# Optimization experiments

Hardware: AMD Instinct MI355X
Metric: run time of the kernel (lower is better)

Reference implementation:

```python
import jax, jax.numpy as jnp
import numpy as np

D = 128          # embed_dim
N = 400000       # rows in each source state buffer (h_bot/c_bot and h_buf/c_buf)
K = 200000       # gathers per source per child side (M = 2*K merge targets)


def setup_inputs() -> dict:
    key = jax.random.key(0)
    ks = jax.random.split(key, 10)
    h_bot = jax.random.normal(ks[0], (N, D), dtype=jnp.float32)
    c_bot = jax.random.normal(ks[1], (N, D), dtype=jnp.float32)
    h_buf = jax.random.normal(ks[2], (N, D), dtype=jnp.float32)
    c_buf = jax.random.normal(ks[3], (N, D), dtype=jnp.float32)
    bot_from_l = jax.random.randint(ks[4], (K,), 0, N, dtype=jnp.int32)
    prev_from_l = jax.random.randint(ks[5], (K,), 0, N, dtype=jnp.int32)
    bot_from_r = jax.random.randint(ks[6], (K,), 0, N, dtype=jnp.int32)
    prev_from_r = jax.random.randint(ks[7], (K,), 0, N, dtype=jnp.int32)
    # BinaryTreeLSTMCell params: 5 gates (i, o, u, f_l, f_r) over [h_l; h_r]
    W = jax.random.normal(ks[8], (2 * D, 5 * D), dtype=jnp.float32) * (1.0 / np.sqrt(2 * D))
    b = jnp.zeros((5 * D,), dtype=jnp.float32)
    return {"h_bot": h_bot, "c_bot": c_bot, "h_buf": h_buf, "c_buf": c_buf,
            "bot_from_l": bot_from_l, "prev_from_l": prev_from_l,
            "bot_from_r": bot_from_r, "prev_from_r": prev_from_r,
            "W": W, "b": b}


def _multi_select(bot_src, prev_src, bot_from, prev_from):
    # multi_index_select with 'to' ids in concat order: gather rows from the two
    # source buffers into the [M, D] merge-target buffer.
    return jnp.concatenate([bot_src[bot_from], prev_src[prev_from]], axis=0)


def _binary_tree_lstm_cell(h_l, c_l, h_r, c_r, W, b):
    # N-ary (N=2) TreeLSTM merge cell, no input x.
    gates = jnp.concatenate([h_l, h_r], axis=1) @ W + b  # [M, 5D]
    i, o, u, f_l, f_r = jnp.split(gates, 5, axis=1)
    c = jax.nn.sigmoid(i) * jnp.tanh(u) \
        + jax.nn.sigmoid(f_l) * c_l + jax.nn.sigmoid(f_r) * c_r
    h = jax.nn.sigmoid(o) * jnp.tanh(c)
    return h, c


def reference(h_bot, c_bot, h_buf, c_buf,
              bot_from_l, prev_from_l, bot_from_r, prev_from_r, W, b):
    # batch_tree_lstm2: tree_state_select gathers for left and right children,
    # then one BinaryTreeLSTMCell merge over all M targets.
    h_l = _multi_select(h_bot, h_buf, bot_from_l, prev_from_l)
    c_l = _multi_select(c_bot, c_buf, bot_from_l, prev_from_l)
    h_r = _multi_select(h_bot, h_buf, bot_from_r, prev_from_r)
    c_r = _multi_select(c_bot, c_buf, bot_from_r, prev_from_r)
    h, c = _binary_tree_lstm_cell(h_l, c_l, h_r, c_r, W, b)
    return jnp.stack([h, c])  # [2, M, D]
```

## Files before the change

kernel.cpp:

```cpp
#include <hip/hip_runtime.h>

typedef __attribute__((ext_vector_type(8))) short short8_t;
typedef __attribute__((ext_vector_type(4))) float f32x4_t;

#define DDIM 128
#define BM   64
#define LDA  264

__device__ __forceinline__ unsigned short f2bf(float x) {
  union { float f; unsigned u; } v; v.f = x;
  unsigned r = v.u + 0x7FFFu + ((v.u >> 16) & 1u);
  return (unsigned short)(r >> 16);
}

__device__ __forceinline__ float sigf(float x) {
  return 1.0f / (1.0f + __expf(-x));
}
__device__ __forceinline__ float tanh_fast(float x) {
  return 2.0f / (1.0f + __expf(-2.0f * x)) - 1.0f;
}

__global__ void convert_w_kernel(const float* __restrict__ W,
                                 unsigned short* __restrict__ Wt,
                                 int twoD, int fiveD) {
  const int c = blockIdx.x;
  const int k = threadIdx.x;
  Wt[c * twoD + k] = f2bf(W[k * fiveD + c]);
}

__global__ __launch_bounds__(512)
void treelstm_fused_kernel(const float* __restrict__ h_bot,
                           const float* __restrict__ c_bot,
                           const float* __restrict__ h_buf,
                           const float* __restrict__ c_buf,
                           const int* __restrict__ idx_bl,
                           const int* __restrict__ idx_pl,
                           const int* __restrict__ idx_br,
                           const int* __restrict__ idx_pr,
                           const float* __restrict__ bias,
                           const unsigned short* __restrict__ Wt,
                           float* __restrict__ out,
                           int K, int M) {
  __shared__ __align__(16) unsigned short A_lds[BM * LDA];

  const int tid   = threadIdx.x;
  const int mbase = blockIdx.x * BM;
  if (mbase >= M) return;

  const int wave = tid >> 6;
  const int lane = tid & 63;
  const int l16  = lane & 15;
  const int lq   = lane >> 4;
  const int d0   = wave * 16 + lq * 4;

  const int r    = tid >> 3;
  const int seg  = tid & 7;
  const int half = seg >> 2;
  const int cs   = seg & 3;
  const int ms   = mbase + r;

  float4 hv[8];
  {
    int hidx; const float* hsrc;
    if (half == 0) {
      if (ms < K) { hidx = idx_bl[ms];     hsrc = h_bot; }
      else        { hidx = idx_pl[ms - K]; hsrc = h_buf; }
    } else {
      if (ms < K) { hidx = idx_br[ms];     hsrc = h_bot; }
      else        { hidx = idx_pr[ms - K]; hsrc = h_buf; }
    }
    const float4* s4 = (const float4*)(hsrc + (size_t)hidx * DDIM);
    #pragma unroll
    for (int q = 0; q < 8; ++q) hv[q] = s4[cs + 4 * q];
  }

  f32x4_t cl[4], cr[4], bs[5];
  int mvec[4];
  #pragma unroll
  for (int mt = 0; mt < 4; ++mt) {
    const int m = mbase + mt * 16 + l16;
    mvec[mt] = m;
    int il, ir; const float *cls, *crs;
    if (m < K) { il = idx_bl[m];     cls = c_bot; }
    else       { il = idx_pl[m - K]; cls = c_buf; }
    if (m < K) { ir = idx_br[m];     crs = c_bot; }
    else       { ir = idx_pr[m - K]; crs = c_buf; }
    cl[mt] = *(const f32x4_t*)(cls + (size_t)il * DDIM + d0);
    cr[mt] = *(const f32x4_t*)(crs + (size_t)ir * DDIM + d0);
  }
  #pragma unroll
  for (int g = 0; g < 5; ++g)
    bs[g] = *(const f32x4_t*)(bias + g * DDIM + d0);

  {
    unsigned short* dst = &A_lds[r * LDA + half * DDIM];
    #pragma unroll
    for (int q = 0; q < 8; ++q) {
      ushort4 w;
      w.x = f2bf(hv[q].x); w.y = f2bf(hv[q].y);
      w.z = f2bf(hv[q].z); w.w = f2bf(hv[q].w);
      *(ushort4*)(dst + (cs + 4 * q) * 4) = w;
    }
  }
  __syncthreads();

  f32x4_t acc[4][5];
  #pragma unroll
  for (int mt = 0; mt < 4; ++mt)
    #pragma unroll
    for (int g = 0; g < 5; ++g) {
      f32x4_t z = {0.0f, 0.0f, 0.0f, 0.0f};
      acc[mt][g] = z;
    }

  const unsigned short* wb = Wt + (size_t)(wave * 16 + l16) * 256 + lq * 8;
  const int ab = l16 * LDA + lq * 8;

  #pragma unroll
  for (int kk = 0; kk < 8; ++kk) {
    const int k0 = kk * 32;
    short8_t wf[5];
    #pragma unroll
    for (int g = 0; g < 5; ++g)
      wf[g] = *(const short8_t*)(wb + (size_t)g * (128 * 256) + k0);
    short8_t hf[4];
    #pragma unroll
    for (int mt = 0; mt < 4; ++mt)
      hf[mt] = *(const short8_t*)(&A_lds[ab + mt * (16 * LDA) + k0]);
    #pragma unroll
    for (int g = 0; g < 5; ++g)
      #pragma unroll
      for (int mt = 0; mt < 4; ++mt)
        acc[mt][g] = __builtin_amdgcn_mfma_f32_16x16x32_bf16(
            wf[g], hf[mt], acc[mt][g], 0, 0, 0);
  }

  float* __restrict__ out_h = out;
  float* __restrict__ out_c = out + (size_t)M * DDIM;

  #pragma unroll
  for (int mt = 0; mt < 4; ++mt) {
    f32x4_t hv4, cv4;
    #pragma unroll
    for (int j = 0; j < 4; ++j) {
      const float gi = acc[mt][0][j] + bs[0][j];
      const float go = acc[mt][1][j] + bs[1][j];
      const float gu = acc[mt][2][j] + bs[2][j];
      const float gl = acc[mt][3][j] + bs[3][j];
      const float gr = acc[mt][4][j] + bs[4][j];
      const float cn = sigf(gi) * tanh_fast(gu)
                     + sigf(gl) * cl[mt][j] + sigf(gr) * cr[mt][j];
      const float hn = sigf(go) * tanh_fast(cn);
      cv4[j] = cn; hv4[j] = hn;
    }
    const size_t off = (size_t)mvec[mt] * DDIM + d0;
    *(f32x4_t*)(out_h + off) = hv4;
    *(f32x4_t*)(out_c + off) = cv4;
  }
}

extern "C" void kernel_launch(void* const* d_in, const int* in_sizes, int n_in,
                              void* d_out, int out_size, void* d_ws, size_t ws_size,
                              hipStream_t stream) {
  const float* h_bot  = (const float*)d_in[0];
  const float* c_bot  = (const float*)d_in[1];
  const float* h_buf  = (const float*)d_in[2];
  const float* c_buf  = (const float*)d_in[3];
  const int*   idx_bl = (const int*)d_in[4];
  const int*   idx_pl = (const int*)d_in[5];
  const int*   idx_br = (const int*)d_in[6];
  const int*   idx_pr = (const int*)d_in[7];
  const float* W      = (const float*)d_in[8];
  const float* bias   = (const float*)d_in[9];

  const int K = in_sizes[4];
  const int M = 2 * K;
  const int fiveD = in_sizes[9];
  const int twoD  = in_sizes[8] / fiveD;

  unsigned short* Wt = (unsigned short*)d_ws;

  hipLaunchKernelGGL(convert_w_kernel, dim3(fiveD), dim3(twoD), 0, stream,
                     W, Wt, twoD, fiveD);

  const int grid = (M + BM - 1) / BM;
  hipLaunchKernelGGL(treelstm_fused_kernel, dim3(grid), dim3(512), 0, stream,
                     h_bot, c_bot, h_buf, c_buf,
                     idx_bl, idx_pl, idx_br, idx_pr,
                     bias, Wt, (float*)d_out, K, M);
}
```

Before: 536.9 us.

## Make fused TreeLSTM kernel persistent with prefetched gathers and swizzled LDS

Replaces the one-tile-per-block launch with a persistent grid of 512 blocks of 256 threads, each looping over 32-row tiles. The next tile's h rows are gathered into registers while the current tile's MFMAs run, then written to LDS after a barrier. The padded LDS layout becomes an XOR-swizzled layout, and sigmoid/tanh use the hardware reciprocal instead of division. The aim is to hide gather latency and cut launch/tail costs. In exchange, the fixed grid of 512 blocks may underfill the GPU, W fragments are reloaded per tile, and each row pays extra barriers.

```diff
diff --git a/kernel.cpp b/kernel.cpp
--- a/kernel.cpp
+++ b/kernel.cpp
@@ -4,8 +4,8 @@
 typedef __attribute__((ext_vector_type(4))) float f32x4_t;
 
 #define DDIM 128
-#define BM   64
-#define LDA  264
+#define BM   32
+#define ROWB 512
 
 __device__ __forceinline__ unsigned short f2bf(float x) {
   union { float f; unsigned u; } v; v.f = x;
@@ -14,10 +14,10 @@
 }
 
 __device__ __forceinline__ float sigf(float x) {
-  return 1.0f / (1.0f + __expf(-x));
+  return __builtin_amdgcn_rcpf(1.0f + __expf(-x));
 }
 __device__ __forceinline__ float tanh_fast(float x) {
-  return 2.0f / (1.0f + __expf(-2.0f * x)) - 1.0f;
+  return 2.0f * __builtin_amdgcn_rcpf(1.0f + __expf(-2.0f * x)) - 1.0f;
 }
 
 __global__ void convert_w_kernel(const float* __restrict__ W,
@@ -28,7 +28,7 @@
   Wt[c * twoD + k] = f2bf(W[k * fiveD + c]);
 }
 
-__global__ __launch_bounds__(512)
+__global__ __launch_bounds__(256)
 void treelstm_fused_kernel(const float* __restrict__ h_bot,
                            const float* __restrict__ c_bot,
                            const float* __restrict__ h_buf,
@@ -40,123 +40,168 @@
                            const float* __restrict__ bias,
                            const unsigned short* __restrict__ Wt,
                            float* __restrict__ out,
-                           int K, int M) {
-  __shared__ __align__(16) unsigned short A_lds[BM * LDA];
-
-  const int tid   = threadIdx.x;
-  const int mbase = blockIdx.x * BM;
-  if (mbase >= M) return;
-
-  const int wave = tid >> 6;
+                           int K, int M, int ntiles) {
+  __shared__ __align__(16) char A_lds[BM * ROWB];
+
+  const int tid = threadIdx.x;
+
+  const int sr    = tid >> 3;
+  const int seg   = tid & 7;
+  const int shalf = seg >> 2;
+  const int scs   = seg & 3;
+  char* const sdst = A_lds + sr * ROWB;
+  const int sswz  = (sr & 7) << 4;
+
+  const int w    = tid >> 6;
   const int lane = tid & 63;
   const int l16  = lane & 15;
   const int lq   = lane >> 4;
-  const int d0   = wave * 16 + lq * 4;
-
-  const int r    = tid >> 3;
-  const int seg  = tid & 7;
-  const int half = seg >> 2;
-  const int cs   = seg & 3;
-  const int ms   = mbase + r;
-
-  float4 hv[8];
+  const int rswz = (l16 & 7) << 4;
+
+  float* const out_h = out;
+  float* const out_c = out + (size_t)M * DDIM;
+
+  int t = blockIdx.x;
+  const int stride = gridDim.x;
+  if (t >= ntiles) return;
+
+#define LOAD_H(tt, hv)                                                   \
+  {                                                                      \
+    const int ms = (tt) * BM + sr;                                       \
+    int hidx = 0; const float* hsrc;                                     \
+    if (shalf == 0) {                                                    \
+      if (ms < K) { hidx = idx_bl[ms]; hsrc = h_bot; }                   \
+      else        { hidx = (ms < M) ? idx_pl[ms - K] : 0; hsrc = h_buf; }\
+    } else {                                                             \
+      if (ms < K) { hidx = idx_br[ms]; hsrc = h_bot; }                   \
+      else        { hidx = (ms < M) ? idx_pr[ms - K] : 0; hsrc = h_buf; }\
+    }                                                                    \
+    const float4* s4 = (const float4*)(hsrc + (size_t)hidx * DDIM);      \
+    _Pragma("unroll")                                                    \
+    for (int q = 0; q < 8; ++q) hv[q] = s4[scs + 4 * q];                 \
+  }
+
+#define WRITE_H(hv)                                                      \
+  {                                                                      \
+    _Pragma("unroll")                                                    \
+    for (int q = 0; q < 8; ++q) {                                        \
+      const int f4i = scs + 4 * q;                                       \
+      ushort4 u;                                                         \
+      u.x = f2bf(hv[q].x); u.y = f2bf(hv[q].y);                          \
+      u.z = f2bf(hv[q].z); u.w = f2bf(hv[q].w);                          \
+      const int byt = (shalf * 256 + f4i * 8) ^ sswz;                    \
+      *(ushort4*)(sdst + byt) = u;                                       \
+    }                                                                    \
+  }
+
   {
-    int hidx; const float* hsrc;
-    if (half == 0) {
-      if (ms < K) { hidx = idx_bl[ms];     hsrc = h_bot; }
-      else        { hidx = idx_pl[ms - K]; hsrc = h_buf; }
-    } else {
-      if (ms < K) { hidx = idx_br[ms];     hsrc = h_bot; }
-      else        { hidx = idx_pr[ms - K]; hsrc = h_buf; }
+    float4 hv[8];
+    LOAD_H(t, hv);
+    WRITE_H(hv);
+  }
+  __syncthreads();
+
+  for (;;) {
+    const int tn = t + stride;
+    const bool more = (tn < ntiles);
+
+    float4 hv2[8];
+    if (more) LOAD_H(tn, hv2);
+
+    const int tb = t * BM;
+    int mvec[2];
+    f32x4_t cl[2][2], cr[2][2];
+    #pragma unroll
+    for (int mt = 0; mt < 2; ++mt) {
+      const int m = tb + mt * 16 + l16;
+      mvec[mt] = m;
+      const int mm = (m < M) ? m : 0;
+      int il, ir; const float *cls, *crs;
+      if (mm < K) { il = idx_bl[mm];     cls = c_bot; }
+      else        { il = idx_pl[mm - K]; cls = c_buf; }
+      if (mm < K) { ir = idx_br[mm];     crs = c_bot; }
+      else        { ir = idx_pr[mm - K]; crs = c_buf; }
+      #pragma unroll
+      for (int dtb = 0; dtb < 2; ++dtb) {
+        const int d0 = dtb * 64 + w * 16 + lq * 4;
+        cl[mt][dtb] = *(const f32x4_t*)(cls + (size_t)il * DDIM + d0);
+        cr[mt][dtb] = *(const f32x4_t*)(crs + (size_t)ir * DDIM + d0);
+      }
     }
-    const float4* s4 = (const float4*)(hsrc + (size_t)hidx * DDIM);
-    #pragma unroll
-    for (int q = 0; q < 8; ++q) hv[q] = s4[cs + 4 * q];
-  }
-
-  f32x4_t cl[4], cr[4], bs[5];
-  int mvec[4];
-  #pragma unroll
-  for (int mt = 0; mt < 4; ++mt) {
-    const int m = mbase + mt * 16 + l16;
-    mvec[mt] = m;
-    int il, ir; const float *cls, *crs;
-    if (m < K) { il = idx_bl[m];     cls = c_bot; }
-    else       { il = idx_pl[m - K]; cls = c_buf; }
-    if (m < K) { ir = idx_br[m];     crs = c_bot; }
-    else       { ir = idx_pr[m - K]; crs = c_buf; }
-    cl[mt] = *(const f32x4_t*)(cls + (size_t)il * DDIM + d0);
-    cr[mt] = *(const f32x4_t*)(crs + (size_t)ir * DDIM + d0);
-  }
-  #pragma unroll
-  for (int g = 0; g < 5; ++g)
-    bs[g] = *(const f32x4_t*)(bias + g * DDIM + d0);
-
-  {
-    unsigned short* dst = &A_lds[r * LDA + half * DDIM];
-    #pragma unroll
-    for (int q = 0; q < 8; ++q) {
-      ushort4 w;
-      w.x = f2bf(hv[q].x); w.y = f2bf(hv[q].y);
-      w.z = f2bf(hv[q].z); w.w = f2bf(hv[q].w);
-      *(ushort4*)(dst + (cs + 4 * q) * 4) = w;
+
+    f32x4_t acc[2][2][5];
+    #pragma unroll
+    for (int mt = 0; mt < 2; ++mt)
+      #pragma unroll
+      for (int dtb = 0; dtb < 2; ++dtb)
+        #pragma unroll
+        for (int g = 0; g < 5; ++g) {
+          f32x4_t z = {0.0f, 0.0f, 0.0f, 0.0f};
+          acc[mt][dtb][g] = z;
+        }
+
+    #pragma unroll
+    for (int kk = 0; kk < 8; ++kk) {
+      short8_t hf[2];
+      #pragma unroll
+      for (int mt = 0; mt < 2; ++mt) {
+        const int byt = (lq * 16 + kk * 64) ^ rswz;
+        hf[mt] = *(const short8_t*)(A_lds + (mt * 16 + l16) * ROWB + byt);
+      }
+      #pragma unroll
+      for (int dtb = 0; dtb < 2; ++dtb)
+        #pragma unroll
+        for (int g = 0; g < 5; ++g) {
+          const int c = g * 128 + dtb * 64 + w * 16 + l16;
+          const short8_t wf =
+              *(const short8_t*)(Wt + (size_t)c * 256 + lq * 8 + kk * 32);
+          #pragma unroll
+          for (int mt = 0; mt < 2; ++mt)
+            acc[mt][dtb][g] = __builtin_amdgcn_mfma_f32_16x16x32_bf16(
+                wf, hf[mt], acc[mt][dtb][g], 0, 0, 0);
+        }
     }
-  }
-  __syncthreads();
-
-  f32x4_t acc[4][5];
-  #pragma unroll
-  for (int mt = 0; mt < 4; ++mt)
-    #pragma unroll
-    for (int g = 0; g < 5; ++g) {
-      f32x4_t z = {0.0f, 0.0f, 0.0f, 0.0f};
-      acc[mt][g] = z;
+
+    __syncthreads();
+    if (more) { WRITE_H(hv2); }
+
+    #pragma unroll
+    for (int mt = 0; mt < 2; ++mt) {
+      if (mvec[mt] < M) {
+        #pragma unroll
+        for (int dtb = 0; dtb < 2; ++dtb) {
+          const int d0 = dtb * 64 + w * 16 + lq * 4;
+          f32x4_t bv[5];
+          #pragma unroll
+          for (int g = 0; g < 5; ++g)
+            bv[g] = *(const f32x4_t*)(bias + g * DDIM + d0);
+          f32x4_t hv4, cv4;
+          #pragma unroll
+          for (int j = 0; j < 4; ++j) {
+            const float gi = acc[mt][dtb][0][j] + bv[0][j];
+            const float go = acc[mt][dtb][1][j] + bv[1][j];
+            const float gu = acc[mt][dtb][2][j] + bv[2][j];
+            const float gl = acc[mt][dtb][3][j] + bv[3][j];
+            const float gr = acc[mt][dtb][4][j] + bv[4][j];
+            const float cn = sigf(gi) * tanh_fast(gu)
+                           + sigf(gl) * cl[mt][dtb][j]
+                           + sigf(gr) * cr[mt][dtb][j];
+            const float hn = sigf(go) * tanh_fast(cn);
+            cv4[j] = cn; hv4[j] = hn;
+          }
+          const size_t off = (size_t)mvec[mt] * DDIM + d0;
+          *(f32x4_t*)(out_h + off) = hv4;
+          *(f32x4_t*)(out_c + off) = cv4;
+        }
+      }
     }
 
-  const unsigned short* wb = Wt + (size_t)(wave * 16 + l16) * 256 + lq * 8;
-  const int ab = l16 * LDA + lq * 8;
-
-  #pragma unroll
-  for (int kk = 0; kk < 8; ++kk) {
-    const int k0 = kk * 32;
-    short8_t wf[5];
-    #pragma unroll
-    for (int g = 0; g < 5; ++g)
-      wf[g] = *(const short8_t*)(wb + (size_t)g * (128 * 256) + k0);
-    short8_t hf[4];
-    #pragma unroll
-    for (int mt = 0; mt < 4; ++mt)
-      hf[mt] = *(const short8_t*)(&A_lds[ab + mt * (16 * LDA) + k0]);
-    #pragma unroll
-    for (int g = 0; g < 5; ++g)
-      #pragma unroll
-      for (int mt = 0; mt < 4; ++mt)
-        acc[mt][g] = __builtin_amdgcn_mfma_f32_16x16x32_bf16(
-            wf[g], hf[mt], acc[mt][g], 0, 0, 0);
-  }
-
-  float* __restrict__ out_h = out;
-  float* __restrict__ out_c = out + (size_t)M * DDIM;
-
-  #pragma unroll
-  for (int mt = 0; mt < 4; ++mt) {
-    f32x4_t hv4, cv4;
-    #pragma unroll
-    for (int j = 0; j < 4; ++j) {
-      const float gi = acc[mt][0][j] + bs[0][j];
-      const float go = acc[mt][1][j] + bs[1][j];
-      const float gu = acc[mt][2][j] + bs[2][j];
-      const float gl = acc[mt][3][j] + bs[3][j];
-      const float gr = acc[mt][4][j] + bs[4][j];
-      const float cn = sigf(gi) * tanh_fast(gu)
-                     + sigf(gl) * cl[mt][j] + sigf(gr) * cr[mt][j];
-      const float hn = sigf(go) * tanh_fast(cn);
-      cv4[j] = cn; hv4[j] = hn;
-    }
-    const size_t off = (size_t)mvec[mt] * DDIM + d0;
-    *(f32x4_t*)(out_h + off) = hv4;
-    *(f32x4_t*)(out_c + off) = cv4;
-  }
+    if (!more) break;
+    __syncthreads();
+    t = tn;
+  }
+#undef LOAD_H
+#undef WRITE_H
 }
 
 extern "C" void kernel_launch(void* const* d_in, const int* in_sizes, int n_in,
@@ -183,9 +228,10 @@
   hipLaunchKernelGGL(convert_w_kernel, dim3(fiveD), dim3(twoD), 0, stream,
                      W, Wt, twoD, fiveD);
 
-  const int grid = (M + BM - 1) / BM;
-  hipLaunchKernelGGL(treelstm_fused_kernel, dim3(grid), dim3(512), 0, stream,
+  const int ntiles = (M + BM - 1) / BM;
+  const int nblocks = 512;
+  hipLaunchKernelGGL(treelstm_fused_kernel, dim3(nblocks), dim3(256), 0, stream,
                      h_bot, c_bot, h_buf, c_buf,
                      idx_bl, idx_pl, idx_br, idx_pr,
-                     bias, Wt, (float*)d_out, K, M);
-}
+                     bias, Wt, (float*)d_out, K, M, ntiles);
+}
```

Result: slower. 562.1 us (+4.7%).

## Persistent double-buffered kernel with direct global-to-LDS gathers of h rows

Applied to the files above, without the earlier changes.

Turns the fused TreeLSTM kernel into a persistent grid of 512 blocks that loop over 32-row tiles. The h rows for the next tile are staged as raw fp32 straight into a swizzled, double-buffered LDS area with global_load_lds while the current tile computes, and the bf16 packing moves to the LDS read path. It also prefetches indices one tile ahead, folds the bias into the accumulator init, and uses hardware reciprocals in sigmoid/tanh. The aim is to hide gather latency behind MFMA work, at the cost of more LDS per block, fp32 staging bandwidth, and truncation rather than round-to-nearest when converting to bf16.

```diff
diff --git a/kernel.cpp b/kernel.cpp
--- a/kernel.cpp
+++ b/kernel.cpp
@@ -2,10 +2,13 @@
 
 typedef __attribute__((ext_vector_type(8))) short short8_t;
 typedef __attribute__((ext_vector_type(4))) float f32x4_t;
-
-#define DDIM 128
-#define BM   64
-#define LDA  264
+typedef __attribute__((ext_vector_type(4))) unsigned int u32x4_t;
+
+#define DDIM  128
+#define BM    32
+#define ROWB  1024
+#define TILEB (BM * ROWB)
+#define NBLK  512
 
 __device__ __forceinline__ unsigned short f2bf(float x) {
   union { float f; unsigned u; } v; v.f = x;
@@ -14,10 +17,20 @@
 }
 
 __device__ __forceinline__ float sigf(float x) {
-  return 1.0f / (1.0f + __expf(-x));
+  return __builtin_amdgcn_rcpf(1.0f + __expf(-x));
 }
 __device__ __forceinline__ float tanh_fast(float x) {
-  return 2.0f / (1.0f + __expf(-2.0f * x)) - 1.0f;
+  return 2.0f * __builtin_amdgcn_rcpf(1.0f + __expf(-2.0f * x)) - 1.0f;
+}
+
+__device__ __forceinline__ unsigned pk2(unsigned lo, unsigned hi) {
+  return (hi & 0xFFFF0000u) | (lo >> 16);
+}
+
+__device__ __forceinline__ void gload_lds16(const float* gp, char* lp) {
+  __builtin_amdgcn_global_load_lds(
+      (const __attribute__((address_space(1))) void*)gp,
+      (__attribute__((address_space(3))) void*)lp, 16, 0, 0);
 }
 
 __global__ void convert_w_kernel(const float* __restrict__ W,
@@ -28,7 +41,7 @@
   Wt[c * twoD + k] = f2bf(W[k * fiveD + c]);
 }
 
-__global__ __launch_bounds__(512)
+__global__ __launch_bounds__(512, 4)
 void treelstm_fused_kernel(const float* __restrict__ h_bot,
                            const float* __restrict__ c_bot,
                            const float* __restrict__ h_buf,
@@ -40,123 +53,159 @@
                            const float* __restrict__ bias,
                            const unsigned short* __restrict__ Wt,
                            float* __restrict__ out,
-                           int K, int M) {
-  __shared__ __align__(16) unsigned short A_lds[BM * LDA];
-
-  const int tid   = threadIdx.x;
-  const int mbase = blockIdx.x * BM;
-  if (mbase >= M) return;
-
-  const int wave = tid >> 6;
+                           int K, int M, int ntiles) {
+  __shared__ __align__(128) char A_lds[2 * TILEB];
+
+  const int tid  = threadIdx.x;
+  const int w    = tid >> 6;
   const int lane = tid & 63;
   const int l16  = lane & 15;
   const int lq   = lane >> 4;
-  const int d0   = wave * 16 + lq * 4;
-
-  const int r    = tid >> 3;
-  const int seg  = tid & 7;
-  const int half = seg >> 2;
-  const int cs   = seg & 3;
-  const int ms   = mbase + r;
-
-  float4 hv[8];
-  {
-    int hidx; const float* hsrc;
-    if (half == 0) {
-      if (ms < K) { hidx = idx_bl[ms];     hsrc = h_bot; }
-      else        { hidx = idx_pl[ms - K]; hsrc = h_buf; }
-    } else {
-      if (ms < K) { hidx = idx_br[ms];     hsrc = h_bot; }
-      else        { hidx = idx_pr[ms - K]; hsrc = h_buf; }
-    }
-    const float4* s4 = (const float4*)(hsrc + (size_t)hidx * DDIM);
-    #pragma unroll
-    for (int q = 0; q < 8; ++q) hv[q] = s4[cs + 4 * q];
-  }
-
-  f32x4_t cl[4], cr[4], bs[5];
-  int mvec[4];
-  #pragma unroll
-  for (int mt = 0; mt < 4; ++mt) {
-    const int m = mbase + mt * 16 + l16;
-    mvec[mt] = m;
-    int il, ir; const float *cls, *crs;
-    if (m < K) { il = idx_bl[m];     cls = c_bot; }
-    else       { il = idx_pl[m - K]; cls = c_buf; }
-    if (m < K) { ir = idx_br[m];     crs = c_bot; }
-    else       { ir = idx_pr[m - K]; crs = c_buf; }
-    cl[mt] = *(const f32x4_t*)(cls + (size_t)il * DDIM + d0);
-    cr[mt] = *(const f32x4_t*)(crs + (size_t)ir * DDIM + d0);
-  }
+  const int d0   = w * 16 + lq * 4;
+  const int w4   = w * 4;
+
+  const int off0 = ((lq * 2) ^ (l16 & 7)) << 4;
+  const int off1 = off0 ^ 16;
+
+  float* const out_h = out;
+  float* const out_c = out + (size_t)M * DDIM;
+
+  const int stride = gridDim.x;
+  int t = blockIdx.x;
+  if (t >= ntiles) return;
+
+  f32x4_t bs[5];
   #pragma unroll
   for (int g = 0; g < 5; ++g)
     bs[g] = *(const f32x4_t*)(bias + g * DDIM + d0);
 
-  {
-    unsigned short* dst = &A_lds[r * LDA + half * DDIM];
+#define LOAD_IQS(tt, dst)                                                  \
+  { _Pragma("unroll")                                                      \
+    for (int q = 0; q < 4; ++q) {                                          \
+      int m = (tt) * BM + w4 + q; if (m >= M) m = M - 1;                   \
+      const int* p;                                                        \
+      if (lane < 32) p = (m < K) ? (idx_bl + m) : (idx_pl + (m - K));      \
+      else           p = (m < K) ? (idx_br + m) : (idx_pr + (m - K));      \
+      dst[q] = *p;                                                         \
+    } }
+
+#define LOAD_ICS(tt, dl, dr)                                               \
+  { _Pragma("unroll")                                                      \
+    for (int mt = 0; mt < 2; ++mt) {                                       \
+      int m = (tt) * BM + mt * 16 + l16; if (m >= M) m = M - 1;            \
+      dl[mt] = (m < K) ? idx_bl[m] : idx_pl[m - K];                        \
+      dr[mt] = (m < K) ? idx_br[m] : idx_pr[m - K];                        \
+    } }
+
+#define STAGE(tt, bufp, iqs)                                               \
+  { _Pragma("unroll")                                                      \
+    for (int q = 0; q < 4; ++q) {                                          \
+      int m = (tt) * BM + w4 + q; if (m >= M) m = M - 1;                   \
+      const int key = (w4 + q) & 7;                                        \
+      const float* hb = (m < K) ? h_bot : h_buf;                           \
+      const float* gp = hb + (size_t)iqs[q] * DDIM + (((lane & 31) ^ key) << 2); \
+      char* lp = (bufp) + (w4 + q) * ROWB;                                 \
+      gload_lds16(gp, lp);                                                 \
+    } }
+
+#define GATHER_C(tt, icl, icr, cl, cr)                                     \
+  { _Pragma("unroll")                                                      \
+    for (int mt = 0; mt < 2; ++mt) {                                       \
+      int m = (tt) * BM + mt * 16 + l16; if (m >= M) m = M - 1;            \
+      const float* cbl = (m < K) ? c_bot : c_buf;                          \
+      cl[mt] = *(const f32x4_t*)(cbl + (size_t)icl[mt] * DDIM + d0);       \
+      cr[mt] = *(const f32x4_t*)(cbl + (size_t)icr[mt] * DDIM + d0);       \
+    } }
+
+  int iqs_cur[4];
+  int icl_cur[2], icr_cur[2], icl_nxt[2], icr_nxt[2];
+
+  LOAD_IQS(t, iqs_cur);
+  LOAD_ICS(t, icl_cur, icr_cur);
+  STAGE(t, A_lds, iqs_cur);
+  if (t + stride < ntiles) LOAD_IQS(t + stride, iqs_cur);
+  __syncthreads();
+
+  int cur = 0;
+  for (;;) {
+    const int tn = t + stride;
+    const bool more = (tn < ntiles);
+    char* const bufc = A_lds + cur * TILEB;
+    char* const bufn = A_lds + (cur ^ 1) * TILEB;
+
+    if (more) STAGE(tn, bufn, iqs_cur);
+
+    f32x4_t cl[2], cr[2];
+    GATHER_C(t, icl_cur, icr_cur, cl, cr);
+
+    if (tn + stride < ntiles) LOAD_IQS(tn + stride, iqs_cur);
+    if (more) LOAD_ICS(tn, icl_nxt, icr_nxt);
+
+    f32x4_t acc[2][5];
     #pragma unroll
-    for (int q = 0; q < 8; ++q) {
-      ushort4 w;
-      w.x = f2bf(hv[q].x); w.y = f2bf(hv[q].y);
-      w.z = f2bf(hv[q].z); w.w = f2bf(hv[q].w);
-      *(ushort4*)(dst + (cs + 4 * q) * 4) = w;
+    for (int mt = 0; mt < 2; ++mt)
+      #pragma unroll
+      for (int g = 0; g < 5; ++g)
+        acc[mt][g] = bs[g];
+
+    #pragma unroll
+    for (int kk = 0; kk < 8; ++kk) {
+      short8_t hf[2];
+      #pragma unroll
+      for (int mt = 0; mt < 2; ++mt) {
+        const char* rb = bufc + (mt * 16 + l16) * ROWB + kk * 128;
+        u32x4_t r0 = *(const u32x4_t*)(rb + off0);
+        u32x4_t r1 = *(const u32x4_t*)(rb + off1);
+        union { unsigned u[4]; short8_t s; } pv;
+        pv.u[0] = pk2(r0.x, r0.y); pv.u[1] = pk2(r0.z, r0.w);
+        pv.u[2] = pk2(r1.x, r1.y); pv.u[3] = pk2(r1.z, r1.w);
+        hf[mt] = pv.s;
+      }
+      #pragma unroll
+      for (int g = 0; g < 5; ++g) {
+        const short8_t wf = *(const short8_t*)(
+            Wt + (size_t)(g * DDIM + w * 16 + l16) * 256 + lq * 8 + kk * 32);
+        #pragma unroll
+        for (int mt = 0; mt < 2; ++mt)
+          acc[mt][g] = __builtin_amdgcn_mfma_f32_16x16x32_bf16(
+              wf, hf[mt], acc[mt][g], 0, 0, 0);
+      }
     }
+
+    #pragma unroll
+    for (int mt = 0; mt < 2; ++mt) {
+      const int m = t * BM + mt * 16 + l16;
+      if (m < M) {
+        f32x4_t hv4, cv4;
+        #pragma unroll
+        for (int j = 0; j < 4; ++j) {
+          const float gi = acc[mt][0][j];
+          const float go = acc[mt][1][j];
+          const float gu = acc[mt][2][j];
+          const float gl = acc[mt][3][j];
+          const float gr = acc[mt][4][j];
+          const float cn = sigf(gi) * tanh_fast(gu)
+                         + sigf(gl) * cl[mt][j] + sigf(gr) * cr[mt][j];
+          const float hn = sigf(go) * tanh_fast(cn);
+          cv4[j] = cn; hv4[j] = hn;
+        }
+        const size_t off = (size_t)m * DDIM + d0;
+        *(f32x4_t*)(out_h + off) = hv4;
+        *(f32x4_t*)(out_c + off) = cv4;
+      }
+    }
+
+    if (!more) break;
+    icl_cur[0] = icl_nxt[0]; icl_cur[1] = icl_nxt[1];
+    icr_cur[0] = icr_nxt[0]; icr_cur[1] = icr_nxt[1];
+    __syncthreads();
+    cur ^= 1;
+    t = tn;
   }
-  __syncthreads();
-
-  f32x4_t acc[4][5];
-  #pragma unroll
-  for (int mt = 0; mt < 4; ++mt)
-    #pragma unroll
-    for (int g = 0; g < 5; ++g) {
-      f32x4_t z = {0.0f, 0.0f, 0.0f, 0.0f};
-      acc[mt][g] = z;
-    }
-
-  const unsigned short* wb = Wt + (size_t)(wave * 16 + l16) * 256 + lq * 8;
-  const int ab = l16 * LDA + lq * 8;
-
-  #pragma unroll
-  for (int kk = 0; kk < 8; ++kk) {
-    const int k0 = kk * 32;
-    short8_t wf[5];
-    #pragma unroll
-    for (int g = 0; g < 5; ++g)
-      wf[g] = *(const short8_t*)(wb + (size_t)g * (128 * 256) + k0);
-    short8_t hf[4];
-    #pragma unroll
-    for (int mt = 0; mt < 4; ++mt)
-      hf[mt] = *(const short8_t*)(&A_lds[ab + mt * (16 * LDA) + k0]);
-    #pragma unroll
-    for (int g = 0; g < 5; ++g)
-      #pragma unroll
-      for (int mt = 0; mt < 4; ++mt)
-        acc[mt][g] = __builtin_amdgcn_mfma_f32_16x16x32_bf16(
-            wf[g], hf[mt], acc[mt][g], 0, 0, 0);
-  }
-
-  float* __restrict__ out_h = out;
-  float* __restrict__ out_c = out + (size_t)M * DDIM;
-
-  #pragma unroll
-  for (int mt = 0; mt < 4; ++mt) {
-    f32x4_t hv4, cv4;
-    #pragma unroll
-    for (int j = 0; j < 4; ++j) {
-      const float gi = acc[mt][0][j] + bs[0][j];
-      const float go = acc[mt][1][j] + bs[1][j];
-      const float gu = acc[mt][2][j] + bs[2][j];
-      const float gl = acc[mt][3][j] + bs[3][j];
-      const float gr = acc[mt][4][j] + bs[4][j];
-      const float cn = sigf(gi) * tanh_fast(gu)
-                     + sigf(gl) * cl[mt][j] + sigf(gr) * cr[mt][j];
-      const float hn = sigf(go) * tanh_fast(cn);
-      cv4[j] = cn; hv4[j] = hn;
-    }
-    const size_t off = (size_t)mvec[mt] * DDIM + d0;
-    *(f32x4_t*)(out_h + off) = hv4;
-    *(f32x4_t*)(out_c + off) = cv4;
-  }
+#undef LOAD_IQS
+#undef LOAD_ICS
+#undef STAGE
+#undef GATHER_C
 }
 
 extern "C" void kernel_launch(void* const* d_in, const int* in_sizes, int n_in,
@@ -183,9 +232,9 @@
   hipLaunchKernelGGL(convert_w_kernel, dim3(fiveD), dim3(twoD), 0, stream,
                      W, Wt, twoD, fiveD);
 
-  const int grid = (M + BM - 1) / BM;
-  hipLaunchKernelGGL(treelstm_fused_kernel, dim3(grid), dim3(512), 0, stream,
+  const int ntiles = (M + BM - 1) / BM;
+  hipLaunchKernelGGL(treelstm_fused_kernel, dim3(NBLK), dim3(512), 0, stream,
                      h_bot, c_bot, h_buf, c_buf,
                      idx_bl, idx_pl, idx_br, idx_pr,
-                     bias, Wt, (float*)d_out, K, M);
-}
+                     bias, Wt, (float*)d_out, K, M, ntiles);
+}
```

New measurement: 1.124 ms. 2.09x slower.

## Shrink row tile to 32, use 256-thread blocks, defer cell-state gathers

Applied to the files above, without the earlier changes.

Row tile drops from 64 to 32 and blocks from 512 to 256 threads with a min-blocks launch bound, so each wave now loops over two 16-column d-blocks. Cell-state gathers move into the epilogue instead of being held in registers across the MFMA loop, and the out-of-range rows are clamped. Sigmoid and tanh now use the hardware reciprocal intrinsic. The aim is lower register pressure and higher occupancy to hide gather latency. The cost is that each block still reads the whole bf16 weight matrix, so weight traffic per output row doubles.

```diff
diff --git a/kernel.cpp b/kernel.cpp
--- a/kernel.cpp
+++ b/kernel.cpp
@@ -4,7 +4,7 @@
 typedef __attribute__((ext_vector_type(4))) float f32x4_t;
 
 #define DDIM 128
-#define BM   64
+#define BM   32
 #define LDA  264
 
 __device__ __forceinline__ unsigned short f2bf(float x) {
@@ -14,10 +14,10 @@
 }
 
 __device__ __forceinline__ float sigf(float x) {
-  return 1.0f / (1.0f + __expf(-x));
+  return __builtin_amdgcn_rcpf(1.0f + __expf(-x));
 }
 __device__ __forceinline__ float tanh_fast(float x) {
-  return 2.0f / (1.0f + __expf(-2.0f * x)) - 1.0f;
+  return 2.0f * __builtin_amdgcn_rcpf(1.0f + __expf(-2.0f * x)) - 1.0f;
 }
 
 __global__ void convert_w_kernel(const float* __restrict__ W,
@@ -28,7 +28,7 @@
   Wt[c * twoD + k] = f2bf(W[k * fiveD + c]);
 }
 
-__global__ __launch_bounds__(512)
+__global__ __launch_bounds__(256, 6)
 void treelstm_fused_kernel(const float* __restrict__ h_bot,
                            const float* __restrict__ c_bot,
                            const float* __restrict__ h_buf,
@@ -45,22 +45,27 @@
 
   const int tid   = threadIdx.x;
   const int mbase = blockIdx.x * BM;
-  if (mbase >= M) return;
 
   const int wave = tid >> 6;
   const int lane = tid & 63;
   const int l16  = lane & 15;
   const int lq   = lane >> 4;
-  const int d0   = wave * 16 + lq * 4;
 
-  const int r    = tid >> 3;
-  const int seg  = tid & 7;
-  const int half = seg >> 2;
-  const int cs   = seg & 3;
-  const int ms   = mbase + r;
+  int il[2], ir[2];
+  #pragma unroll
+  for (int mt = 0; mt < 2; ++mt) {
+    int m = mbase + mt * 16 + l16; if (m >= M) m = M - 1;
+    il[mt] = (m < K) ? idx_bl[m] : idx_pl[m - K];
+    ir[mt] = (m < K) ? idx_br[m] : idx_pr[m - K];
+  }
 
-  float4 hv[8];
   {
+    const int r    = tid >> 3;
+    const int seg  = tid & 7;
+    const int half = seg >> 2;
+    const int cs   = seg & 3;
+    int ms = mbase + r; if (ms >= M) ms = M - 1;
+
     int hidx; const float* hsrc;
     if (half == 0) {
       if (ms < K) { hidx = idx_bl[ms];     hsrc = h_bot; }
@@ -70,92 +75,85 @@
       else        { hidx = idx_pr[ms - K]; hsrc = h_buf; }
     }
     const float4* s4 = (const float4*)(hsrc + (size_t)hidx * DDIM);
-    #pragma unroll
-    for (int q = 0; q < 8; ++q) hv[q] = s4[cs + 4 * q];
-  }
-
-  f32x4_t cl[4], cr[4], bs[5];
-  int mvec[4];
-  #pragma unroll
-  for (int mt = 0; mt < 4; ++mt) {
-    const int m = mbase + mt * 16 + l16;
-    mvec[mt] = m;
-    int il, ir; const float *cls, *crs;
-    if (m < K) { il = idx_bl[m];     cls = c_bot; }
-    else       { il = idx_pl[m - K]; cls = c_buf; }
-    if (m < K) { ir = idx_br[m];     crs = c_bot; }
-    else       { ir = idx_pr[m - K]; crs = c_buf; }
-    cl[mt] = *(const f32x4_t*)(cls + (size_t)il * DDIM + d0);
-    cr[mt] = *(const f32x4_t*)(crs + (size_t)ir * DDIM + d0);
-  }
-  #pragma unroll
-  for (int g = 0; g < 5; ++g)
-    bs[g] = *(const f32x4_t*)(bias + g * DDIM + d0);
-
-  {
     unsigned short* dst = &A_lds[r * LDA + half * DDIM];
     #pragma unroll
     for (int q = 0; q < 8; ++q) {
-      ushort4 w;
-      w.x = f2bf(hv[q].x); w.y = f2bf(hv[q].y);
-      w.z = f2bf(hv[q].z); w.w = f2bf(hv[q].w);
-      *(ushort4*)(dst + (cs + 4 * q) * 4) = w;
+      const int f4i = cs + 4 * q;
+      float4 v = s4[f4i];
+      ushort4 u;
+      u.x = f2bf(v.x); u.y = f2bf(v.y); u.z = f2bf(v.z); u.w = f2bf(v.w);
+      *(ushort4*)(dst + f4i * 4) = u;
     }
   }
   __syncthreads();
 
-  f32x4_t acc[4][5];
+  float* const out_h = out;
+  float* const out_c = out + (size_t)M * DDIM;
+
   #pragma unroll
-  for (int mt = 0; mt < 4; ++mt)
+  for (int p = 0; p < 2; ++p) {
+    const int dblk = wave + 4 * p;
+    const int d0   = dblk * 16 + lq * 4;
+
+    f32x4_t acc[2][5];
     #pragma unroll
-    for (int g = 0; g < 5; ++g) {
-      f32x4_t z = {0.0f, 0.0f, 0.0f, 0.0f};
-      acc[mt][g] = z;
+    for (int mt = 0; mt < 2; ++mt)
+      #pragma unroll
+      for (int g = 0; g < 5; ++g) {
+        f32x4_t z = {0.0f, 0.0f, 0.0f, 0.0f};
+        acc[mt][g] = z;
+      }
+
+    const unsigned short* wb = Wt + (size_t)(dblk * 16 + l16) * 256 + lq * 8;
+    const int ab = l16 * LDA + lq * 8;
+
+    #pragma unroll
+    for (int kk = 0; kk < 8; ++kk) {
+      const int k0 = kk * 32;
+      short8_t hf[2];
+      #pragma unroll
+      for (int mt = 0; mt < 2; ++mt)
+        hf[mt] = *(const short8_t*)(&A_lds[ab + mt * (16 * LDA) + k0]);
+      #pragma unroll
+      for (int g = 0; g < 5; ++g) {
+        const short8_t wf = *(const short8_t*)(wb + (size_t)g * (128 * 256) + k0);
+        #pragma unroll
+        for (int mt = 0; mt < 2; ++mt)
+          acc[mt][g] = __builtin_amdgcn_mfma_f32_16x16x32_bf16(
+              wf, hf[mt], acc[mt][g], 0, 0, 0);
+      }
     }
 
-  const unsigned short* wb = Wt + (size_t)(wave * 16 + l16) * 256 + lq * 8;
-  const int ab = l16 * LDA + lq * 8;
-
-  #pragma unroll
-  for (int kk = 0; kk < 8; ++kk) {
-    const int k0 = kk * 32;
-    short8_t wf[5];
+    f32x4_t bs[5];
     #pragma unroll
     for (int g = 0; g < 5; ++g)
-      wf[g] = *(const short8_t*)(wb + (size_t)g * (128 * 256) + k0);
-    short8_t hf[4];
+      bs[g] = *(const f32x4_t*)(bias + g * DDIM + d0);
+
     #pragma unroll
-    for (int mt = 0; mt < 4; ++mt)
-      hf[mt] = *(const short8_t*)(&A_lds[ab + mt * (16 * LDA) + k0]);
-    #pragma unroll
-    for (int g = 0; g < 5; ++g)
-      #pragma unroll
-      for (int mt = 0; mt < 4; ++mt)
-        acc[mt][g] = __builtin_amdgcn_mfma_f32_16x16x32_bf16(
-            wf[g], hf[mt], acc[mt][g], 0, 0, 0);
-  }
-
-  float* __restrict__ out_h = out;
-  float* __restrict__ out_c = out + (size_t)M * DDIM;
-
-  #pragma unroll
-  for (int mt = 0; mt < 4; ++mt) {
-    f32x4_t hv4, cv4;
-    #pragma unroll
-    for (int j = 0; j < 4; ++j) {
-      const float gi = acc[mt][0][j] + bs[0][j];
-      const float go = acc[mt][1][j] + bs[1][j];
-      const float gu = acc[mt][2][j] + bs[2][j];
-      const float gl = acc[mt][3][j] + bs[3][j];
-      const float gr = acc[mt][4][j] + bs[4][j];
-      const float cn = sigf(gi) * tanh_fast(gu)
-                     + sigf(gl) * cl[mt][j] + sigf(gr) * cr[mt][j];
-      const float hn = sigf(go) * tanh_fast(cn);
-      cv4[j] = cn; hv4[j] = hn;
+    for (int mt = 0; mt < 2; ++mt) {
+      const int m = mbase + mt * 16 + l16;
+      if (m < M) {
+        const float* cls = (m < K) ? c_bot : c_buf;
+        const f32x4_t clv = *(const f32x4_t*)(cls + (size_t)il[mt] * DDIM + d0);
+        const f32x4_t crv = *(const f32x4_t*)(cls + (size_t)ir[mt] * DDIM + d0);
+        f32x4_t hv4, cv4;
+        #pragma unroll
+        for (int j = 0; j < 4; ++j) {
+          const float gi = acc[mt][0][j] + bs[0][j];
+          const float go = acc[mt][1][j] + bs[1][j];
+          const float gu = acc[mt][2][j] + bs[2][j];
+          const float gl = acc[mt][3][j] + bs[3][j];
+          const float gr = acc[mt][4][j] + bs[4][j];
+          const float cn = sigf(gi) * tanh_fast(gu)
+                         + sigf(gl) * clv[j] + sigf(gr) * crv[j];
+          const float hn = sigf(go) * tanh_fast(cn);
+          cv4[j] = cn; hv4[j] = hn;
+        }
+        const size_t off = (size_t)m * DDIM + d0;
+        *(f32x4_t*)(out_h + off) = hv4;
+        *(f32x4_t*)(out_c + off) = cv4;
+      }
     }
-    const size_t off = (size_t)mvec[mt] * DDIM + d0;
-    *(f32x4_t*)(out_h + off) = hv4;
-    *(f32x4_t*)(out_c + off) = cv4;
   }
 }
 
@@ -184,7 +182,7 @@
                      W, Wt, twoD, fiveD);
 
   const int grid = (M + BM - 1) / BM;
-  hipLaunchKernelGGL(treelstm_fused_kernel, dim3(grid), dim3(512), 0, stream,
+  hipLaunchKernelGGL(treelstm_fused_kernel, dim3(grid), dim3(256), 0, stream,
                      h_bot, c_bot, h_buf, c_buf,
                      idx_bl, idx_pl, idx_br, idx_pr,
                      bias, Wt, (float*)d_out, K, M);
```

New measurement: 739.8 us. 1.38x slower.
